# Performance work log

Hardware: AMD Instinct MI355X
Metric: run time of the kernel (lower is better)

## Reference

```python
import jax, jax.numpy as jnp
import numpy as np

D_MODEL, D_STATE, D_CONV, DT_RANK = 512, 64, 4, 32


def setup_inputs() -> dict:
    key = jax.random.key(0)
    ks = jax.random.split(key, 8)
    Bsz, L = 2, 2048
    s = lambda k, shape: jax.random.normal(k, shape, jnp.float32) * 0.02
    return {
        "x": jax.random.normal(ks[0], (Bsz, L, D_MODEL), jnp.float32),
        "in_proj_w": s(ks[1], (D_MODEL, 2 * D_MODEL)),
        "in_proj_b": jnp.zeros((2 * D_MODEL,), jnp.float32),
        "conv_w": s(ks[2], (D_MODEL, 1, D_CONV)),  # depthwise: [C_out, C_in/groups=1, K]
        "conv_b": jnp.zeros((D_MODEL,), jnp.float32),
        "x_proj_w": s(ks[3], (D_MODEL, DT_RANK + 2 * D_STATE)),
        "x_proj_b": jnp.zeros((DT_RANK + 2 * D_STATE,), jnp.float32),
        "dt_proj_w": s(ks[4], (DT_RANK, D_MODEL)),
        "dt_proj_b": jnp.zeros((D_MODEL,), jnp.float32),
        "A_log": jnp.log(jnp.broadcast_to(
            jnp.arange(1, D_STATE + 1, dtype=jnp.float32), (D_MODEL, D_STATE))),
        "B_param": jax.random.normal(ks[5], (D_MODEL, D_STATE), jnp.float32),
        "C_param": jax.random.normal(ks[6], (D_MODEL, D_STATE), jnp.float32),
        "D_param": jnp.ones((D_MODEL,), jnp.float32),
    }


def reference(x, in_proj_w, in_proj_b, conv_w, conv_b, x_proj_w, x_proj_b,
              dt_proj_w, dt_proj_b, A_log, B_param, C_param, D_param):
    Bsz, L, _ = x.shape
    # in_proj -> split into (x, z)
    xz = x @ in_proj_w + in_proj_b                       # [B, L, 2D]
    xc, z = jnp.split(xz, 2, axis=-1)                    # each [B, L, D]
    # depthwise causal conv1d, padding=K-1 both sides, truncate to L (as in torch)
    y = jax.lax.conv_general_dilated(
        xc.transpose(0, 2, 1), conv_w, window_strides=(1,),
        padding=[(D_CONV - 1, D_CONV - 1)],
        dimension_numbers=("NCH", "OIH", "NCH"),
        feature_group_count=D_MODEL)                     # [B, D, L+K-1]
    xc = (y + conv_b[None, :, None])[:, :, :L].transpose(0, 2, 1)  # [B, L, D]
    # selective parameters
    xp = xc @ x_proj_w + x_proj_b                        # [B, L, dt_rank + 2N]
    dt, Bp, Cp = jnp.split(xp, [DT_RANK, DT_RANK + D_STATE], axis=-1)
    dt = jax.nn.softplus(dt @ dt_proj_w + dt_proj_b)     # [B, L, D]
    A = -jnp.exp(A_log)                                  # [D, N]

    def step(h, ins):
        dt_t, Bp_t, Cp_t, u_t = ins                      # [B,D],[B,N],[B,N],[B,D]
        A_d = jnp.exp(dt_t[..., None] * A)               # [B, D, N]
        B_d = dt_t[..., None] * (B_param * Bp_t[:, None, :])
        h = A_d * h + B_d * u_t[..., None]               # [B, D, N]
        y_t = jnp.sum((C_param * Cp_t[:, None, :]) * h, axis=-1)  # [B, D]
        return h, y_t

    h0 = jnp.zeros((Bsz, D_MODEL, D_STATE), x.dtype)
    xs = (dt.transpose(1, 0, 2), Bp.transpose(1, 0, 2),
          Cp.transpose(1, 0, 2), xc.transpose(1, 0, 2))
    _, ys = jax.lax.scan(step, h0, xs)                   # ys: [L, B, D]
    y = ys.transpose(1, 0, 2) + D_param * xc             # skip connection
    return y * jax.nn.silu(z)                            # gated output [B, L, D]
```

## Files before the change

### kernel.cpp

```cpp
#include <hip/hip_runtime.h>
#include <hip/hip_bf16.h>

#define BSZ 2
#define SEQL 2048
#define DM 512
#define DST 64
#define DCONV 4
#define DTR 32
#define NROWS (BSZ * SEQL)

#define NC 32
#define CL 64

#define XPD_LD 640

typedef unsigned short u16;
typedef short bf16x8 __attribute__((ext_vector_type(8)));
typedef float f32x4 __attribute__((ext_vector_type(4)));

__device__ __forceinline__ u16 f2bf(float f) {
  unsigned u = __float_as_uint(f);
  return (u16)((u + 0x7FFFu + ((u >> 16) & 1u)) >> 16);
}
__device__ __forceinline__ float bf2f(u16 h) {
  return __uint_as_float(((unsigned)h) << 16);
}

__device__ __forceinline__ void gload_lds16(const u16* g, u16* l) {
  __builtin_amdgcn_global_load_lds(
      (const __attribute__((address_space(1))) void*)(const void*)g,
      (__attribute__((address_space(3))) void*)(void*)l, 16, 0, 0);
}

__global__ __launch_bounds__(256) void split_x_kernel(
    const float* __restrict__ x, u16* __restrict__ hi, u16* __restrict__ lo) {
  int idx = (blockIdx.x * 256 + threadIdx.x) * 4;
  float4 v = *(const float4*)(x + idx);
  ushort4 h, l;
  h.x = f2bf(v.x); l.x = f2bf(v.x - bf2f(h.x));
  h.y = f2bf(v.y); l.y = f2bf(v.y - bf2f(h.y));
  h.z = f2bf(v.z); l.z = f2bf(v.z - bf2f(h.z));
  h.w = f2bf(v.w); l.w = f2bf(v.w - bf2f(h.w));
  *(ushort4*)(hi + idx) = h;
  *(ushort4*)(lo + idx) = l;
}

__global__ __launch_bounds__(256) void split_w_kernel(
    const float* __restrict__ W, u16* __restrict__ Wt_hi,
    u16* __restrict__ Wt_lo) {
  __shared__ u16 shi[32][33], slo[32][33];
  const int n0 = blockIdx.x * 32;
  const int k0 = blockIdx.y * 32;
  const int i = threadIdx.x >> 5;
  const int j = threadIdx.x & 31;
#pragma unroll
  for (int r = 0; r < 4; ++r) {
    int k = i + r * 8;
    float v = W[(size_t)(k0 + k) * 1024 + n0 + j];
    u16 h = f2bf(v);
    shi[k][j] = h;
    slo[k][j] = f2bf(v - bf2f(h));
  }
  __syncthreads();
#pragma unroll
  for (int r = 0; r < 4; ++r) {
    int n = i + r * 8;
    Wt_hi[(size_t)(n0 + n) * 512 + k0 + j] = shi[j][n];
    Wt_lo[(size_t)(n0 + n) * 512 + k0 + j] = slo[j][n];
  }
}

__global__ __launch_bounds__(256) void w_combine_kernel(
    const float* __restrict__ xw, const float* __restrict__ dw,
    u16* __restrict__ Wt_hi, u16* __restrict__ Wt_lo) {
  int idx = blockIdx.x * 256 + threadIdx.x;
  int r = idx >> 9;
  int k = idx & 511;
  float v;
  if (r < 128) {
    v = xw[(size_t)k * 160 + 32 + r];
  } else {
    int d = r - 128;
    float s = 0.f;
#pragma unroll
    for (int j = 0; j < DTR; ++j) s += xw[(size_t)k * 160 + j] * dw[(size_t)j * DM + d];
    v = s;
  }
  u16 h = f2bf(v);
  Wt_hi[idx] = h;
  Wt_lo[idx] = f2bf(v - bf2f(h));
}

__global__ __launch_bounds__(256) void bias_combine_kernel(
    const float* __restrict__ xb, const float* __restrict__ dw,
    const float* __restrict__ db, float* __restrict__ bias_c) {
  int r = blockIdx.x * 256 + threadIdx.x;
  if (r >= 640) return;
  float v;
  if (r < 128) {
    v = xb[32 + r];
  } else {
    int d = r - 128;
    float s = db[d];
#pragma unroll
    for (int j = 0; j < DTR; ++j) s += xb[j] * dw[(size_t)j * DM + d];
    v = s;
  }
  bias_c[r] = v;
}

__global__ __launch_bounds__(256) void mfma_split_gemm(
    const u16* __restrict__ A_hi, const u16* __restrict__ A_lo,
    const u16* __restrict__ Bt_hi, const u16* __restrict__ Bt_lo,
    const float* __restrict__ bias, float* __restrict__ C,
    int ldc, int act_from) {
  __shared__ alignas(16) u16 sAh[4096], sAl[4096], sBh[4096], sBl[4096];

  const int lane = threadIdx.x & 63;
  const int wv = threadIdx.x >> 6;
  const int bm = blockIdx.y * 128;
  const int bn = blockIdx.x * 128;
  const int fr = lane & 15;
  const int q = lane >> 4;

  const int st_rowc = lane >> 2;
  const int st_qd = lane & 3;

  const bf16x8 *pAh[4], *pAl[4], *pBh[4], *pBl[4];
#pragma unroll
  for (int t = 0; t < 4; ++t) {
    int ra = (wv >> 1) * 64 + t * 16 + fr;
    int ea = ra * 32 + ((q ^ ((ra >> 1) & 3)) * 8);
    pAh[t] = (const bf16x8*)(sAh + ea);
    pAl[t] = (const bf16x8*)(sAl + ea);
    int rb = (wv & 1) * 64 + t * 16 + fr;
    int eb = rb * 32 + ((q ^ ((rb >> 1) & 3)) * 8);
    pBh[t] = (const bf16x8*)(sBh + eb);
    pBl[t] = (const bf16x8*)(sBl + eb);
  }

  f32x4 zero = {0.f, 0.f, 0.f, 0.f};
  f32x4 acc[4][4];
#pragma unroll
  for (int i = 0; i < 4; ++i)
#pragma unroll
    for (int j = 0; j < 4; ++j) acc[i][j] = zero;

  auto stage = [&](int k0) {
#pragma unroll
    for (int i = 0; i < 2; ++i) {
      int c = wv + i * 4;
      int row = c * 16 + st_rowc;
      int qs = st_qd ^ ((row >> 1) & 3);
      size_t ga = (size_t)(bm + row) * 512 + k0 + qs * 8;
      size_t gb = (size_t)(bn + row) * 512 + k0 + qs * 8;
      gload_lds16(A_hi + ga, sAh + c * 512);
      gload_lds16(A_lo + ga, sAl + c * 512);
      gload_lds16(Bt_hi + gb, sBh + c * 512);
      gload_lds16(Bt_lo + gb, sBl + c * 512);
    }
  };

  stage(0);
  for (int kt = 0; kt < 16; ++kt) {
    __syncthreads();
    bf16x8 ah[4], al[4], bh[4], bl[4];
#pragma unroll
    for (int t = 0; t < 4; ++t) {
      ah[t] = *pAh[t];
      al[t] = *pAl[t];
      bh[t] = *pBh[t];
      bl[t] = *pBl[t];
    }
    __syncthreads();
    if (kt < 15) stage((kt + 1) * 32);
#pragma unroll
    for (int mi = 0; mi < 4; ++mi)
#pragma unroll
      for (int nj = 0; nj < 4; ++nj) {
        f32x4 a = acc[mi][nj];
        a = __builtin_amdgcn_mfma_f32_16x16x32_bf16(al[mi], bh[nj], a, 0, 0, 0);
        a = __builtin_amdgcn_mfma_f32_16x16x32_bf16(ah[mi], bl[nj], a, 0, 0, 0);
        a = __builtin_amdgcn_mfma_f32_16x16x32_bf16(ah[mi], bh[nj], a, 0, 0, 0);
        acc[mi][nj] = a;
      }
  }

  const bool act = (bn >= act_from);
#pragma unroll
  for (int mi = 0; mi < 4; ++mi) {
#pragma unroll
    for (int nj = 0; nj < 4; ++nj) {
      int row = bm + (wv >> 1) * 64 + mi * 16 + q * 4;
      int col = bn + (wv & 1) * 64 + nj * 16 + fr;
      float bs = bias[col];
#pragma unroll
      for (int e = 0; e < 4; ++e) {
        float v = acc[mi][nj][e] + bs;
        if (act) v = (v > 20.f) ? v : log1pf(expf(v));
        C[(size_t)(row + e) * ldc + col] = v;
      }
    }
  }
}

__global__ __launch_bounds__(256) void conv_split_kernel(
    const float* __restrict__ xz, const float* __restrict__ w,
    const float* __restrict__ cb, float* __restrict__ xc,
    u16* __restrict__ hi, u16* __restrict__ lo) {
  int idx = blockIdx.x * blockDim.x + threadIdx.x;
  if (idx >= NROWS * DM) return;
  int d = idx & (DM - 1);
  int t = (idx >> 9) & (SEQL - 1);
  int b = idx >> 20;
  float acc = cb[d];
#pragma unroll
  for (int k = 0; k < DCONV; ++k) {
    int ts = t + k - (DCONV - 1);
    if (ts >= 0)
      acc += w[d * DCONV + k] * xz[((size_t)(b * SEQL + ts)) * (2 * DM) + d];
  }
  xc[idx] = acc;
  u16 h = f2bf(acc);
  hi[idx] = h;
  lo[idx] = f2bf(acc - bf2f(h));
}

__global__ __launch_bounds__(256) void scan_phase1(
    const float* __restrict__ xpd, const float* __restrict__ xc,
    const float* __restrict__ A_log, const float* __restrict__ Bpar,
    float* __restrict__ hout, float* __restrict__ sdt_arr) {
  const int lane = threadIdx.x & 63;
  const int wid = (blockIdx.x << 2) + (threadIdx.x >> 6);
  const int ch = wid >> 5;
  const int c = wid & (NC - 1);
  const int b = ch >> 9;
  const int d = ch & (DM - 1);
  const int n = lane;

  const float aq = -__expf(A_log[d * DST + n]) * 1.44269504f;
  const float bpn = Bpar[d * DST + n];
  float h = 0.f, sdt = 0.f;

  const size_t row0 = (size_t)b * SEQL + (size_t)c * CL;
  const float* dtp = xpd + row0 * XPD_LD + 128 + d;
  const float* up = xc + row0 * DM + d;
  const float* bp = xpd + row0 * XPD_LD + n;

  for (int t0 = 0; t0 < CL; t0 += 4) {
    float dtv[4], uv[4], bpt[4];
#pragma unroll
    for (int j = 0; j < 4; ++j) {
      dtv[j] = dtp[(size_t)(t0 + j) * XPD_LD];
      uv[j] = up[(size_t)(t0 + j) * DM];
      bpt[j] = bp[(size_t)(t0 + j) * XPD_LD];
    }
#pragma unroll
    for (int j = 0; j < 4; ++j) {
      float Ad = exp2f(dtv[j] * aq);
      h = Ad * h + (bpn * bpt[j]) * (dtv[j] * uv[j]);
      sdt += dtv[j];
    }
  }
  hout[(size_t)wid * DST + n] = h;
  if (lane == 0) sdt_arr[wid] = sdt;
}

__global__ __launch_bounds__(256) void scan_phase2(
    const float* __restrict__ A_log, float* __restrict__ hout,
    const float* __restrict__ sdt_arr) {
  const int lane = threadIdx.x & 63;
  const int ch = (blockIdx.x << 2) + (threadIdx.x >> 6);
  const int d = ch & (DM - 1);
  const float aq = -__expf(A_log[d * DST + lane]) * 1.44269504f;

  float tmp[NC], pa[NC];
#pragma unroll
  for (int c = 0; c < NC; ++c) {
    tmp[c] = hout[((size_t)ch * NC + c) * DST + lane];
    pa[c] = exp2f(aq * sdt_arr[ch * NC + c]);
  }
  float h = 0.f;
#pragma unroll
  for (int c = 0; c < NC; ++c) {
    hout[((size_t)ch * NC + c) * DST + lane] = h;
    h = pa[c] * h + tmp[c];
  }
}

__global__ __launch_bounds__(256) void scan_phase3(
    const float* __restrict__ xpd, const float* __restrict__ xc,
    const float* __restrict__ xz,
    const float* __restrict__ A_log, const float* __restrict__ Bpar,
    const float* __restrict__ Cpar, const float* __restrict__ Dpar,
    const float* __restrict__ hin, float* __restrict__ out) {
  __shared__ float W[4][16][68];

  const int lane = threadIdx.x & 63;
  const int wave = threadIdx.x >> 6;
  const int wid = (blockIdx.x << 2) + wave;
  const int ch = wid >> 5;
  const int c = wid & (NC - 1);
  const int b = ch >> 9;
  const int d = ch & (DM - 1);
  const int n = lane;

  const float aq = -__expf(A_log[d * DST + n]) * 1.44269504f;
  const float bpn = Bpar[d * DST + n];
  const float cpn = Cpar[d * DST + n];
  const float Dd = Dpar[d];
  float h = hin[(size_t)wid * DST + n];

  const size_t row0 = (size_t)b * SEQL + (size_t)c * CL;
  const float* dtp = xpd + row0 * XPD_LD + 128 + d;
  const float* up = xc + row0 * DM + d;
  const float* bp = xpd + row0 * XPD_LD + n;
  const float* cp = xpd + row0 * XPD_LD + 64 + n;

  const int tt = lane & 15;
  const int q = lane >> 4;

  for (int t0 = 0; t0 < CL; t0 += 16) {
#pragma unroll
    for (int g = 0; g < 16; g += 4) {
      float dtv[4], uv[4], bpt[4], cpt[4];
#pragma unroll
      for (int j = 0; j < 4; ++j) {
        size_t t = (size_t)(t0 + g + j);
        dtv[j] = dtp[t * XPD_LD];
        uv[j] = up[t * DM];
        bpt[j] = bp[t * XPD_LD];
        cpt[j] = cp[t * XPD_LD];
      }
#pragma unroll
      for (int j = 0; j < 4; ++j) {
        float Ad = exp2f(dtv[j] * aq);
        h = Ad * h + (bpn * bpt[j]) * (dtv[j] * uv[j]);
        W[wave][g + j][n] = (cpn * cpt[j]) * h;
      }
    }
    const float4* wr = (const float4*)&W[wave][tt][q * 16];
    float s = 0.f;
#pragma unroll
    for (int k2 = 0; k2 < 4; ++k2) {
      float4 v = wr[k2];
      s += (v.x + v.y) + (v.z + v.w);
    }
    s += __shfl_xor(s, 16, 64);
    s += __shfl_xor(s, 32, 64);
    if (lane < 16) {
      size_t t = (size_t)(t0 + lane);
      float u = up[t * DM];
      float zz = xz[(row0 + t) * (2 * DM) + DM + d];
      float y = s + Dd * u;
      float sil = zz / (1.f + __expf(-zz));
      out[(row0 + t) * DM + d] = y * sil;
    }
  }
}

extern "C" void kernel_launch(void* const* d_in, const int* in_sizes, int n_in,
                              void* d_out, int out_size, void* d_ws,
                              size_t ws_size, hipStream_t stream) {
  const float* x = (const float*)d_in[0];
  const float* in_proj_w = (const float*)d_in[1];
  const float* in_proj_b = (const float*)d_in[2];
  const float* conv_w = (const float*)d_in[3];
  const float* conv_b = (const float*)d_in[4];
  const float* x_proj_w = (const float*)d_in[5];
  const float* x_proj_b = (const float*)d_in[6];
  const float* dt_proj_w = (const float*)d_in[7];
  const float* dt_proj_b = (const float*)d_in[8];
  const float* A_log = (const float*)d_in[9];
  const float* B_param = (const float*)d_in[10];
  const float* C_param = (const float*)d_in[11];
  const float* D_param = (const float*)d_in[12];
  float* out = (float*)d_out;

  float* ws = (float*)d_ws;
  float* xz = ws;
  float* xc = xz + (size_t)NROWS * 2 * DM;
  float* xpd = xc + (size_t)NROWS * DM;
  float* hout = xpd + (size_t)NROWS * XPD_LD;
  float* sdt = hout + (size_t)BSZ * DM * NC * DST;
  float* bias_c = sdt + (size_t)BSZ * DM * NC;
  u16* A_hi = (u16*)(bias_c + 1024);
  u16* A_lo = A_hi + (size_t)NROWS * DM;
  u16* Wt_in_hi = A_lo + (size_t)NROWS * DM;
  u16* Wt_in_lo = Wt_in_hi + (size_t)1024 * 512;
  u16* Wt_c_hi = Wt_in_lo + (size_t)1024 * 512;
  u16* Wt_c_lo = Wt_c_hi + (size_t)640 * 512;

  hipLaunchKernelGGL(split_x_kernel, dim3((NROWS * DM) / (256 * 4)), dim3(256),
                     0, stream, x, A_hi, A_lo);
  hipLaunchKernelGGL(split_w_kernel, dim3(32, 16), dim3(256), 0, stream,
                     in_proj_w, Wt_in_hi, Wt_in_lo);
  hipLaunchKernelGGL(w_combine_kernel, dim3((640 * 512) / 256), dim3(256), 0,
                     stream, x_proj_w, dt_proj_w, Wt_c_hi, Wt_c_lo);
  hipLaunchKernelGGL(bias_combine_kernel, dim3(3), dim3(256), 0, stream,
                     x_proj_b, dt_proj_w, dt_proj_b, bias_c);

  hipLaunchKernelGGL(mfma_split_gemm, dim3(1024 / 128, NROWS / 128),
                     dim3(256), 0, stream, A_hi, A_lo, Wt_in_hi, Wt_in_lo,
                     in_proj_b, xz, 1024, 1 << 30);

  {
    int total = NROWS * DM;
    hipLaunchKernelGGL(conv_split_kernel, dim3((total + 255) / 256), dim3(256),
                       0, stream, xz, conv_w, conv_b, xc, A_hi, A_lo);
  }
  hipLaunchKernelGGL(mfma_split_gemm, dim3(640 / 128, NROWS / 128),
                     dim3(256), 0, stream, A_hi, A_lo, Wt_c_hi, Wt_c_lo,
                     bias_c, xpd, XPD_LD, 128);

  {
    dim3 grid((BSZ * DM * NC) / 4);
    hipLaunchKernelGGL(scan_phase1, grid, dim3(256), 0, stream,
                       xpd, xc, A_log, B_param, hout, sdt);
    hipLaunchKernelGGL(scan_phase2, dim3((BSZ * DM) / 4), dim3(256), 0, stream,
                       A_log, hout, sdt);
    hipLaunchKernelGGL(scan_phase3, grid, dim3(256), 0, stream,
                       xpd, xc, xz, A_log, B_param, C_param, D_param,
                       hout, out);
  }
}
```

Baseline: 305.6 us.

## Add dedicated xpd GEMM with LDS-resident B and split softplus into separate kernel

Replaces the generic split-bf16 GEMM for the x_proj/dt_proj stage with a kernel using 128x64 tiles. It loads the full 64x512 weight slice into LDS once and reads A fragments straight from global memory. The softplus epilogue moves into a separate elementwise kernel, so both GEMMs lose the runtime activation branch. The change doubles the block count for the 640-wide GEMM for better occupancy, at the cost of 128KB of LDS per block, uncached global A loads, and one extra kernel launch with an extra read and write of the dt columns.

```diff
diff --git a/kernel.cpp b/kernel.cpp
--- a/kernel.cpp
+++ b/kernel.cpp
@@ -112,8 +112,7 @@
 __global__ __launch_bounds__(256) void mfma_split_gemm(
     const u16* __restrict__ A_hi, const u16* __restrict__ A_lo,
     const u16* __restrict__ Bt_hi, const u16* __restrict__ Bt_lo,
-    const float* __restrict__ bias, float* __restrict__ C,
-    int ldc, int act_from) {
+    const float* __restrict__ bias, float* __restrict__ C) {
   __shared__ alignas(16) u16 sAh[4096], sAl[4096], sBh[4096], sBl[4096];
 
   const int lane = threadIdx.x & 63;
@@ -186,7 +185,6 @@
       }
   }
 
-  const bool act = (bn >= act_from);
 #pragma unroll
   for (int mi = 0; mi < 4; ++mi) {
 #pragma unroll
@@ -195,13 +193,109 @@
       int col = bn + (wv & 1) * 64 + nj * 16 + fr;
       float bs = bias[col];
 #pragma unroll
-      for (int e = 0; e < 4; ++e) {
-        float v = acc[mi][nj][e] + bs;
-        if (act) v = (v > 20.f) ? v : log1pf(expf(v));
-        C[(size_t)(row + e) * ldc + col] = v;
+      for (int e = 0; e < 4; ++e)
+        C[(size_t)(row + e) * 1024 + col] = acc[mi][nj][e] + bs;
+    }
+  }
+}
+
+__global__ __launch_bounds__(256) void xpd_gemm_kernel(
+    const u16* __restrict__ A_hi, const u16* __restrict__ A_lo,
+    const u16* __restrict__ Bt_hi, const u16* __restrict__ Bt_lo,
+    const float* __restrict__ bias, float* __restrict__ C) {
+  __shared__ alignas(16) u16 sBh[64 * 512];
+  __shared__ alignas(16) u16 sBl[64 * 512];
+
+  const int lane = threadIdx.x & 63;
+  const int wv = threadIdx.x >> 6;
+  const int wr = wv >> 1;
+  const int wc = wv & 1;
+  const int bm = blockIdx.y * 128;
+  const int bn = blockIdx.x * 64;
+  const int fr = lane & 15;
+  const int q = lane >> 4;
+
+  {
+    const int r0 = wv * 16;
+#pragma unroll
+    for (int i = 0; i < 16; ++i) {
+      int r = r0 + i;
+      size_t g = (size_t)(bn + r) * 512 + (size_t)(lane ^ (r & 7)) * 8;
+      gload_lds16(Bt_hi + g, sBh + r * 512);
+      gload_lds16(Bt_lo + g, sBl + r * 512);
+    }
+  }
+  __syncthreads();
+
+  size_t arow[4];
+#pragma unroll
+  for (int mi = 0; mi < 4; ++mi)
+    arow[mi] = (size_t)(bm + wr * 64 + mi * 16 + fr) * 512;
+  int bcol[2];
+#pragma unroll
+  for (int nj = 0; nj < 2; ++nj) bcol[nj] = wc * 32 + nj * 16 + fr;
+
+  f32x4 zero = {0.f, 0.f, 0.f, 0.f};
+  f32x4 acc[4][2];
+#pragma unroll
+  for (int i = 0; i < 4; ++i) {
+    acc[i][0] = zero;
+    acc[i][1] = zero;
+  }
+
+#pragma unroll 4
+  for (int kt = 0; kt < 16; ++kt) {
+    bf16x8 ah[4], al[4], bh[2], bl[2];
+    const int kc = kt * 4 + q;
+#pragma unroll
+    for (int nj = 0; nj < 2; ++nj) {
+      int off = bcol[nj] * 512 + ((kc ^ (bcol[nj] & 7)) * 8);
+      bh[nj] = *(const bf16x8*)(sBh + off);
+      bl[nj] = *(const bf16x8*)(sBl + off);
+    }
+#pragma unroll
+    for (int mi = 0; mi < 4; ++mi) {
+      size_t ga = arow[mi] + kt * 32 + q * 8;
+      ah[mi] = *(const bf16x8*)(A_hi + ga);
+      al[mi] = *(const bf16x8*)(A_lo + ga);
+    }
+#pragma unroll
+    for (int mi = 0; mi < 4; ++mi)
+#pragma unroll
+      for (int nj = 0; nj < 2; ++nj) {
+        f32x4 a = acc[mi][nj];
+        a = __builtin_amdgcn_mfma_f32_16x16x32_bf16(al[mi], bh[nj], a, 0, 0, 0);
+        a = __builtin_amdgcn_mfma_f32_16x16x32_bf16(ah[mi], bl[nj], a, 0, 0, 0);
+        a = __builtin_amdgcn_mfma_f32_16x16x32_bf16(ah[mi], bh[nj], a, 0, 0, 0);
+        acc[mi][nj] = a;
       }
-    }
-  }
+  }
+
+#pragma unroll
+  for (int mi = 0; mi < 4; ++mi) {
+#pragma unroll
+    for (int nj = 0; nj < 2; ++nj) {
+      int row = bm + wr * 64 + mi * 16 + q * 4;
+      int col = bn + wc * 32 + nj * 16 + fr;
+      float bs = bias[col];
+#pragma unroll
+      for (int e = 0; e < 4; ++e)
+        C[(size_t)(row + e) * XPD_LD + col] = acc[mi][nj][e] + bs;
+    }
+  }
+}
+
+__global__ __launch_bounds__(256) void softplus_kernel(float* __restrict__ xpd) {
+  int idx = blockIdx.x * 256 + threadIdx.x;
+  int row = idx >> 7;
+  int cq = (idx & 127) * 4;
+  float* p = xpd + (size_t)row * XPD_LD + 128 + cq;
+  float4 v = *(float4*)p;
+  v.x = (v.x > 20.f) ? v.x : log1pf(expf(v.x));
+  v.y = (v.y > 20.f) ? v.y : log1pf(expf(v.y));
+  v.z = (v.z > 20.f) ? v.z : log1pf(expf(v.z));
+  v.w = (v.w > 20.f) ? v.w : log1pf(expf(v.w));
+  *(float4*)p = v;
 }
 
 __global__ __launch_bounds__(256) void conv_split_kernel(
@@ -402,16 +496,18 @@
 
   hipLaunchKernelGGL(mfma_split_gemm, dim3(1024 / 128, NROWS / 128),
                      dim3(256), 0, stream, A_hi, A_lo, Wt_in_hi, Wt_in_lo,
-                     in_proj_b, xz, 1024, 1 << 30);
+                     in_proj_b, xz);
 
   {
     int total = NROWS * DM;
     hipLaunchKernelGGL(conv_split_kernel, dim3((total + 255) / 256), dim3(256),
                        0, stream, xz, conv_w, conv_b, xc, A_hi, A_lo);
   }
-  hipLaunchKernelGGL(mfma_split_gemm, dim3(640 / 128, NROWS / 128),
+  hipLaunchKernelGGL(xpd_gemm_kernel, dim3(640 / 64, NROWS / 128),
                      dim3(256), 0, stream, A_hi, A_lo, Wt_c_hi, Wt_c_lo,
-                     bias_c, xpd, XPD_LD, 128);
+                     bias_c, xpd);
+  hipLaunchKernelGGL(softplus_kernel, dim3((NROWS * 512) / (256 * 4)),
+                     dim3(256), 0, stream, xpd);
 
   {
     dim3 grid((BSZ * DM * NC) / 4);
```

Result: faster. 263.6 us (-13.7%).

## Keep weight tile resident in LDS, interleave B/C columns, repack dt and dt*u

Applied to the files above, without the earlier changes.

The split-bf16 GEMM now loads its full 64-column weight panel into LDS once and streams A fragments straight from global memory, which removes the per-k double syncthreads staging. The x_proj output columns for B and C are interleaved so the scan kernels fetch both with one float2 load. A new repack kernel applies softplus and writes dt and dt*u transposed per channel, giving the scan phases contiguous loads instead of loads strided by the row width. The costs are 128KB of LDS per GEMM block, which limits occupancy, uncached direct A loads, and one extra pass over a large buffer.

```diff
diff --git a/kernel.cpp b/kernel.cpp
--- a/kernel.cpp
+++ b/kernel.cpp
@@ -78,7 +78,8 @@
   int k = idx & 511;
   float v;
   if (r < 128) {
-    v = xw[(size_t)k * 160 + 32 + r];
+    int nn = r >> 1;
+    v = (r & 1) ? xw[(size_t)k * 160 + 96 + nn] : xw[(size_t)k * 160 + 32 + nn];
   } else {
     int d = r - 128;
     float s = 0.f;
@@ -98,7 +99,8 @@
   if (r >= 640) return;
   float v;
   if (r < 128) {
-    v = xb[32 + r];
+    int nn = r >> 1;
+    v = (r & 1) ? xb[96 + nn] : xb[32 + nn];
   } else {
     int d = r - 128;
     float s = db[d];
@@ -109,75 +111,70 @@
   bias_c[r] = v;
 }
 
-__global__ __launch_bounds__(256) void mfma_split_gemm(
+__global__ __launch_bounds__(256) void resident_gemm_kernel(
     const u16* __restrict__ A_hi, const u16* __restrict__ A_lo,
     const u16* __restrict__ Bt_hi, const u16* __restrict__ Bt_lo,
-    const float* __restrict__ bias, float* __restrict__ C,
-    int ldc, int act_from) {
-  __shared__ alignas(16) u16 sAh[4096], sAl[4096], sBh[4096], sBl[4096];
+    const float* __restrict__ bias, float* __restrict__ C, int ldc) {
+  __shared__ alignas(16) u16 sBh[64 * 512];
+  __shared__ alignas(16) u16 sBl[64 * 512];
 
   const int lane = threadIdx.x & 63;
   const int wv = threadIdx.x >> 6;
+  const int wr = wv >> 1;
+  const int wc = wv & 1;
   const int bm = blockIdx.y * 128;
-  const int bn = blockIdx.x * 128;
+  const int bn = blockIdx.x * 64;
   const int fr = lane & 15;
   const int q = lane >> 4;
 
-  const int st_rowc = lane >> 2;
-  const int st_qd = lane & 3;
-
-  const bf16x8 *pAh[4], *pAl[4], *pBh[4], *pBl[4];
-#pragma unroll
-  for (int t = 0; t < 4; ++t) {
-    int ra = (wv >> 1) * 64 + t * 16 + fr;
-    int ea = ra * 32 + ((q ^ ((ra >> 1) & 3)) * 8);
-    pAh[t] = (const bf16x8*)(sAh + ea);
-    pAl[t] = (const bf16x8*)(sAl + ea);
-    int rb = (wv & 1) * 64 + t * 16 + fr;
-    int eb = rb * 32 + ((q ^ ((rb >> 1) & 3)) * 8);
-    pBh[t] = (const bf16x8*)(sBh + eb);
-    pBl[t] = (const bf16x8*)(sBl + eb);
-  }
+  {
+    const int r0 = wv * 16;
+#pragma unroll
+    for (int i = 0; i < 16; ++i) {
+      int r = r0 + i;
+      size_t g = (size_t)(bn + r) * 512 + (size_t)(lane ^ (r & 7)) * 8;
+      gload_lds16(Bt_hi + g, sBh + r * 512);
+      gload_lds16(Bt_lo + g, sBl + r * 512);
+    }
+  }
+  __syncthreads();
+
+  size_t arow[4];
+#pragma unroll
+  for (int mi = 0; mi < 4; ++mi)
+    arow[mi] = (size_t)(bm + wr * 64 + mi * 16 + fr) * 512;
+  int bcol[2];
+#pragma unroll
+  for (int nj = 0; nj < 2; ++nj) bcol[nj] = wc * 32 + nj * 16 + fr;
 
   f32x4 zero = {0.f, 0.f, 0.f, 0.f};
-  f32x4 acc[4][4];
-#pragma unroll
-  for (int i = 0; i < 4; ++i)
-#pragma unroll
-    for (int j = 0; j < 4; ++j) acc[i][j] = zero;
-
-  auto stage = [&](int k0) {
-#pragma unroll
-    for (int i = 0; i < 2; ++i) {
-      int c = wv + i * 4;
-      int row = c * 16 + st_rowc;
-      int qs = st_qd ^ ((row >> 1) & 3);
-      size_t ga = (size_t)(bm + row) * 512 + k0 + qs * 8;
-      size_t gb = (size_t)(bn + row) * 512 + k0 + qs * 8;
-      gload_lds16(A_hi + ga, sAh + c * 512);
-      gload_lds16(A_lo + ga, sAl + c * 512);
-      gload_lds16(Bt_hi + gb, sBh + c * 512);
-      gload_lds16(Bt_lo + gb, sBl + c * 512);
-    }
-  };
-
-  stage(0);
+  f32x4 acc[4][2];
+#pragma unroll
+  for (int i = 0; i < 4; ++i) {
+    acc[i][0] = zero;
+    acc[i][1] = zero;
+  }
+
+#pragma unroll 4
   for (int kt = 0; kt < 16; ++kt) {
-    __syncthreads();
-    bf16x8 ah[4], al[4], bh[4], bl[4];
-#pragma unroll
-    for (int t = 0; t < 4; ++t) {
-      ah[t] = *pAh[t];
-      al[t] = *pAl[t];
-      bh[t] = *pBh[t];
-      bl[t] = *pBl[t];
-    }
-    __syncthreads();
-    if (kt < 15) stage((kt + 1) * 32);
+    bf16x8 ah[4], al[4], bh[2], bl[2];
+    const int kc = kt * 4 + q;
+#pragma unroll
+    for (int nj = 0; nj < 2; ++nj) {
+      int off = bcol[nj] * 512 + ((kc ^ (bcol[nj] & 7)) * 8);
+      bh[nj] = *(const bf16x8*)(sBh + off);
+      bl[nj] = *(const bf16x8*)(sBl + off);
+    }
+#pragma unroll
+    for (int mi = 0; mi < 4; ++mi) {
+      size_t ga = arow[mi] + kt * 32 + q * 8;
+      ah[mi] = *(const bf16x8*)(A_hi + ga);
+      al[mi] = *(const bf16x8*)(A_lo + ga);
+    }
 #pragma unroll
     for (int mi = 0; mi < 4; ++mi)
 #pragma unroll
-      for (int nj = 0; nj < 4; ++nj) {
+      for (int nj = 0; nj < 2; ++nj) {
         f32x4 a = acc[mi][nj];
         a = __builtin_amdgcn_mfma_f32_16x16x32_bf16(al[mi], bh[nj], a, 0, 0, 0);
         a = __builtin_amdgcn_mfma_f32_16x16x32_bf16(ah[mi], bl[nj], a, 0, 0, 0);
@@ -186,20 +183,16 @@
       }
   }
 
-  const bool act = (bn >= act_from);
 #pragma unroll
   for (int mi = 0; mi < 4; ++mi) {
 #pragma unroll
-    for (int nj = 0; nj < 4; ++nj) {
-      int row = bm + (wv >> 1) * 64 + mi * 16 + q * 4;
-      int col = bn + (wv & 1) * 64 + nj * 16 + fr;
+    for (int nj = 0; nj < 2; ++nj) {
+      int row = bm + wr * 64 + mi * 16 + q * 4;
+      int col = bn + wc * 32 + nj * 16 + fr;
       float bs = bias[col];
 #pragma unroll
-      for (int e = 0; e < 4; ++e) {
-        float v = acc[mi][nj][e] + bs;
-        if (act) v = (v > 20.f) ? v : log1pf(expf(v));
-        C[(size_t)(row + e) * ldc + col] = v;
-      }
+      for (int e = 0; e < 4; ++e)
+        C[(size_t)(row + e) * ldc + col] = acc[mi][nj][e] + bs;
     }
   }
 }
@@ -226,8 +219,36 @@
   lo[idx] = f2bf(acc - bf2f(h));
 }
 
+__global__ __launch_bounds__(256) void repack_kernel(
+    const float* __restrict__ xpd, const float* __restrict__ xc,
+    float2* __restrict__ du2) {
+  __shared__ float2 ldu[32][33];
+  const int tid = threadIdx.x;
+  const int r0 = blockIdx.x * 32;
+  const int d0 = blockIdx.y * 32;
+  const int lr = tid >> 5;
+  const int ld = tid & 31;
+#pragma unroll
+  for (int p = 0; p < 4; ++p) {
+    int rr = lr + p * 8;
+    size_t row = (size_t)(r0 + rr);
+    float dt = xpd[row * XPD_LD + 128 + d0 + ld];
+    dt = (dt > 20.f) ? dt : log1pf(expf(dt));
+    float u = xc[row * DM + d0 + ld];
+    ldu[rr][ld] = make_float2(dt, dt * u);
+  }
+  __syncthreads();
+  const int b = r0 >> 11;
+  const int t0 = r0 & (SEQL - 1);
+  const int dr = tid >> 3;
+  const int tc = (tid & 7) * 4;
+  float2* dst = du2 + ((size_t)(b * DM + d0 + dr)) * SEQL + t0 + tc;
+#pragma unroll
+  for (int k = 0; k < 4; ++k) dst[k] = ldu[tc + k][dr];
+}
+
 __global__ __launch_bounds__(256) void scan_phase1(
-    const float* __restrict__ xpd, const float* __restrict__ xc,
+    const float* __restrict__ xpd, const float2* __restrict__ du2,
     const float* __restrict__ A_log, const float* __restrict__ Bpar,
     float* __restrict__ hout, float* __restrict__ sdt_arr) {
   const int lane = threadIdx.x & 63;
@@ -243,23 +264,21 @@
   float h = 0.f, sdt = 0.f;
 
   const size_t row0 = (size_t)b * SEQL + (size_t)c * CL;
-  const float* dtp = xpd + row0 * XPD_LD + 128 + d;
-  const float* up = xc + row0 * DM + d;
-  const float* bp = xpd + row0 * XPD_LD + n;
+  const float2* dup = du2 + (size_t)ch * SEQL + (size_t)c * CL;
+  const float2* bcp = (const float2*)xpd + row0 * 320 + n;
 
   for (int t0 = 0; t0 < CL; t0 += 4) {
-    float dtv[4], uv[4], bpt[4];
+    float2 duv[4], bc[4];
 #pragma unroll
     for (int j = 0; j < 4; ++j) {
-      dtv[j] = dtp[(size_t)(t0 + j) * XPD_LD];
-      uv[j] = up[(size_t)(t0 + j) * DM];
-      bpt[j] = bp[(size_t)(t0 + j) * XPD_LD];
+      duv[j] = dup[t0 + j];
+      bc[j] = bcp[(size_t)(t0 + j) * 320];
     }
 #pragma unroll
     for (int j = 0; j < 4; ++j) {
-      float Ad = exp2f(dtv[j] * aq);
-      h = Ad * h + (bpn * bpt[j]) * (dtv[j] * uv[j]);
-      sdt += dtv[j];
+      float Ad = exp2f(duv[j].x * aq);
+      h = Ad * h + (bpn * bc[j].x) * duv[j].y;
+      sdt += duv[j].x;
     }
   }
   hout[(size_t)wid * DST + n] = h;
@@ -289,8 +308,8 @@
 }
 
 __global__ __launch_bounds__(256) void scan_phase3(
-    const float* __restrict__ xpd, const float* __restrict__ xc,
-    const float* __restrict__ xz,
+    const float* __restrict__ xpd, const float2* __restrict__ du2,
+    const float* __restrict__ xc, const float* __restrict__ xz,
     const float* __restrict__ A_log, const float* __restrict__ Bpar,
     const float* __restrict__ Cpar, const float* __restrict__ Dpar,
     const float* __restrict__ hin, float* __restrict__ out) {
@@ -312,10 +331,9 @@
   float h = hin[(size_t)wid * DST + n];
 
   const size_t row0 = (size_t)b * SEQL + (size_t)c * CL;
-  const float* dtp = xpd + row0 * XPD_LD + 128 + d;
+  const float2* dup = du2 + (size_t)ch * SEQL + (size_t)c * CL;
+  const float2* bcp = (const float2*)xpd + row0 * 320 + n;
   const float* up = xc + row0 * DM + d;
-  const float* bp = xpd + row0 * XPD_LD + n;
-  const float* cp = xpd + row0 * XPD_LD + 64 + n;
 
   const int tt = lane & 15;
   const int q = lane >> 4;
@@ -323,20 +341,17 @@
   for (int t0 = 0; t0 < CL; t0 += 16) {
 #pragma unroll
     for (int g = 0; g < 16; g += 4) {
-      float dtv[4], uv[4], bpt[4], cpt[4];
+      float2 duv[4], bc[4];
 #pragma unroll
       for (int j = 0; j < 4; ++j) {
-        size_t t = (size_t)(t0 + g + j);
-        dtv[j] = dtp[t * XPD_LD];
-        uv[j] = up[t * DM];
-        bpt[j] = bp[t * XPD_LD];
-        cpt[j] = cp[t * XPD_LD];
+        duv[j] = dup[t0 + g + j];
+        bc[j] = bcp[(size_t)(t0 + g + j) * 320];
       }
 #pragma unroll
       for (int j = 0; j < 4; ++j) {
-        float Ad = exp2f(dtv[j] * aq);
-        h = Ad * h + (bpn * bpt[j]) * (dtv[j] * uv[j]);
-        W[wave][g + j][n] = (cpn * cpt[j]) * h;
+        float Ad = exp2f(duv[j].x * aq);
+        h = Ad * h + (bpn * bc[j].x) * duv[j].y;
+        W[wave][g + j][n] = (cpn * bc[j].y) * h;
       }
     }
     const float4* wr = (const float4*)&W[wave][tt][q * 16];
@@ -384,7 +399,8 @@
   float* hout = xpd + (size_t)NROWS * XPD_LD;
   float* sdt = hout + (size_t)BSZ * DM * NC * DST;
   float* bias_c = sdt + (size_t)BSZ * DM * NC;
-  u16* A_hi = (u16*)(bias_c + 1024);
+  float2* du2 = (float2*)(bias_c + 1024);
+  u16* A_hi = (u16*)(du2 + (size_t)NROWS * DM);
   u16* A_lo = A_hi + (size_t)NROWS * DM;
   u16* Wt_in_hi = A_lo + (size_t)NROWS * DM;
   u16* Wt_in_lo = Wt_in_hi + (size_t)1024 * 512;
@@ -400,27 +416,30 @@
   hipLaunchKernelGGL(bias_combine_kernel, dim3(3), dim3(256), 0, stream,
                      x_proj_b, dt_proj_w, dt_proj_b, bias_c);
 
-  hipLaunchKernelGGL(mfma_split_gemm, dim3(1024 / 128, NROWS / 128),
+  hipLaunchKernelGGL(resident_gemm_kernel, dim3(1024 / 64, NROWS / 128),
                      dim3(256), 0, stream, A_hi, A_lo, Wt_in_hi, Wt_in_lo,
-                     in_proj_b, xz, 1024, 1 << 30);
+                     in_proj_b, xz, 1024);
 
   {
     int total = NROWS * DM;
     hipLaunchKernelGGL(conv_split_kernel, dim3((total + 255) / 256), dim3(256),
                        0, stream, xz, conv_w, conv_b, xc, A_hi, A_lo);
   }
-  hipLaunchKernelGGL(mfma_split_gemm, dim3(640 / 128, NROWS / 128),
+  hipLaunchKernelGGL(resident_gemm_kernel, dim3(640 / 64, NROWS / 128),
                      dim3(256), 0, stream, A_hi, A_lo, Wt_c_hi, Wt_c_lo,
-                     bias_c, xpd, XPD_LD, 128);
+                     bias_c, xpd, XPD_LD);
+
+  hipLaunchKernelGGL(repack_kernel, dim3(NROWS / 32, DM / 32), dim3(256), 0,
+                     stream, xpd, xc, du2);
 
   {
     dim3 grid((BSZ * DM * NC) / 4);
     hipLaunchKernelGGL(scan_phase1, grid, dim3(256), 0, stream,
-                       xpd, xc, A_log, B_param, hout, sdt);
+                       xpd, du2, A_log, B_param, hout, sdt);
     hipLaunchKernelGGL(scan_phase2, dim3((BSZ * DM) / 4), dim3(256), 0, stream,
                        A_log, hout, sdt);
     hipLaunchKernelGGL(scan_phase3, grid, dim3(256), 0, stream,
-                       xpd, xc, xz, A_log, B_param, C_param, D_param,
+                       xpd, du2, xc, xz, A_log, B_param, C_param, D_param,
                        hout, out);
   }
 }
```

New measurement: 326.4 us. +6.8%, slower.
